# Optimization experiments

Hardware: AMD Instinct MI355X
Metric: run time of the kernel (lower is better)

## Reference

```python
import jax, jax.numpy as jnp
import numpy as np

VOCAB = 32000
EMBED = 256
UNITS = 1024
BATCH = 16
SEQ = 128


def setup_inputs() -> dict:
    key = jax.random.key(0)
    ks = jax.random.split(key, 7)
    scale_in = 1.0 / np.sqrt(EMBED + UNITS)
    return {
        "inputs": jax.random.randint(ks[0], (BATCH, SEQ), 0, VOCAB, dtype=jnp.int64),
        "emb": jax.random.normal(ks[1], (VOCAB, EMBED), dtype=jnp.float32) * 0.05,
        "W": jax.random.normal(ks[2], (EMBED, 4 * UNITS), dtype=jnp.float32) * scale_in,
        "U": jax.random.normal(ks[3], (UNITS, 4 * UNITS), dtype=jnp.float32) * scale_in,
        "b": jnp.zeros((4 * UNITS,), dtype=jnp.float32),
        "Wc": jax.random.normal(ks[5], (UNITS, VOCAB), dtype=jnp.float32) * (1.0 / np.sqrt(UNITS)),
        "bc": jnp.zeros((VOCAB,), dtype=jnp.float32),
    }


def reference(inputs, emb, W, U, b, Wc, bc):
    # Embedding lookup: [B, T] -> [B, T, E]
    x = emb[inputs]
    B, T, E = x.shape
    H = U.shape[0]

    def step(carry, xt):
        h, c = carry
        # fused gate pre-activations: [B, 4H]
        z = xt @ W + h @ U + b
        i, f, g, o = jnp.split(z, 4, axis=-1)
        c_new = jax.nn.sigmoid(f) * c + jax.nn.sigmoid(i) * jnp.tanh(g)
        h_new = jax.nn.sigmoid(o) * jnp.tanh(c_new)
        return (h_new, c_new), h_new

    h0 = jnp.zeros((B, H), dtype=x.dtype)
    c0 = jnp.zeros((B, H), dtype=x.dtype)
    (h, c), hs = jax.lax.scan(step, (h0, c0), jnp.swapaxes(x, 0, 1))  # hs: [T, B, H]

    out = jnp.swapaxes(hs, 0, 1).reshape(-1, H)  # [B*T, H]
    logits = out @ Wc + bc                        # [B*T, vocab]
    return logits
```

## Files before the change

### kernel.cpp

```cpp
#include <hip/hip_runtime.h>
#include <hip/hip_bf16.h>
#include <math.h>


#define VOCAB 32000
#define EMBED 256
#define UNITS 1024
#define GATES 4096
#define BATCH 16
#define SEQ 128
#define NB 64

using s16x8 = __attribute__((ext_vector_type(8))) short;
using f16x8 = __attribute__((ext_vector_type(8))) _Float16;
using f32x4 = __attribute__((ext_vector_type(4))) float;

__device__ __forceinline__ unsigned short f16_bits(float x) {
    _Float16 h = (_Float16)x;
    return __builtin_bit_cast(unsigned short, h);
}
__device__ __forceinline__ float f16_f32(unsigned short b) {
    return (float)__builtin_bit_cast(_Float16, b);
}
__device__ __forceinline__ int swz_e(int r, int k) {
    return (r * 64 + k) ^ ((((r & 7) ^ ((r >> 2) & 7))) << 3);
}
__device__ __forceinline__ unsigned long long ld_u64(const unsigned long long* p) {
    return __hip_atomic_load(p, __ATOMIC_RELAXED, __HIP_MEMORY_SCOPE_AGENT);
}
__device__ __forceinline__ unsigned poison_u64(unsigned long long v) {
    return (unsigned)((unsigned)v == 0xFFFFFFFFu) |
           (unsigned)((unsigned)(v >> 32) == 0xFFFFFFFFu);
}

__global__ void __launch_bounds__(256) k_prep(
    const float* __restrict__ U,
    unsigned short* __restrict__ ub_hi,
    unsigned short* __restrict__ ub_lo,
    const int* __restrict__ inputs,
    const float* __restrict__ emb,
    const float* __restrict__ W,
    const float* __restrict__ bias,
    float* __restrict__ xWb) {
    __shared__ __align__(16) char smem_raw[65536];
    const int tid = threadIdx.x;

    if (blockIdx.x < 256) {
        float* lds_u = (float*)smem_raw;
        const int ct = blockIdx.x;
        for (int k = tid; k < 1024; k += 256) {
            const float4* src = (const float4*)(U + (size_t)k * GATES + ct * 16);
            float4* dst = (float4*)(&lds_u[k * 16]);
            dst[0] = src[0]; dst[1] = src[1]; dst[2] = src[2]; dst[3] = src[3];
        }
        __syncthreads();
        const int lane = tid & 63;
        const int coll = lane & 15;
        const int kg = lane >> 4;
        for (int kt = (tid >> 6); kt < 32; kt += 4) {
            const int ks = kt * 32 + kg * 8;
            unsigned short h8[8], l8[8];
#pragma unroll
            for (int e = 0; e < 8; ++e) {
                float v = lds_u[(ks + e) * 16 + coll];
                unsigned short hb = f16_bits(v);
                h8[e] = hb;
                l8[e] = f16_bits(v - f16_f32(hb));
            }
            size_t o = (((size_t)ct * 32 + kt) * 64 + lane) * 8;
            *(s16x8*)(ub_hi + o) = *(const s16x8*)h8;
            *(s16x8*)(ub_lo + o) = *(const s16x8*)l8;
        }
        return;
    }

    const int eb = blockIdx.x - 256;
    const int t   = eb >> 4;
    const int col = (eb & 15) * 256 + tid;
    float (*xs)[EMBED] = (float (*)[EMBED])smem_raw;
    int* toks = (int*)(smem_raw + 16384);
    if (tid < BATCH)
        toks[tid] = inputs[tid * SEQ + t];
    __syncthreads();
    for (int r = 0; r < BATCH; ++r)
        xs[r][tid] = emb[(size_t)toks[r] * EMBED + tid];
    __syncthreads();
    float acc[BATCH];
#pragma unroll
    for (int r = 0; r < BATCH; ++r) acc[r] = 0.f;
    for (int k0 = 0; k0 < EMBED; k0 += 4) {
        float4 xv[BATCH];
#pragma unroll
        for (int r = 0; r < BATCH; ++r)
            xv[r] = *(const float4*)(&xs[r][k0]);
#pragma unroll
        for (int e = 0; e < 4; ++e) {
            float w = W[(size_t)(k0 + e) * GATES + col];
#pragma unroll
            for (int r = 0; r < BATCH; ++r)
                acc[r] += ((const float*)&xv[r])[e] * w;
        }
    }
    const float bb = bias[col];
#pragma unroll
    for (int r = 0; r < BATCH; ++r)
        xWb[((size_t)t * BATCH + r) * GATES + col] = acc[r] + bb;
}

__global__ void __launch_bounds__(512, 2) k_fused(
    const unsigned short* __restrict__ ub_hi,
    const unsigned short* __restrict__ ub_lo,
    const float* __restrict__ xWb,
    unsigned short* __restrict__ hsl,
    const float* __restrict__ Wc,
    const float* __restrict__ bc,
    float* __restrict__ out) {
    __shared__ __align__(16) char smem_raw[32768];
    const int tid  = threadIdx.x;
    const int lane = tid & 63;
    const int w    = tid >> 6;

    if (blockIdx.x < NB) {
        __builtin_amdgcn_s_setprio(1);
        float (*zpart)[4][256] = (float (*)[4][256])smem_raw;
        const int bid = blockIdx.x;
        const int j0  = bid * 16;

        const int b_own  = (tid >> 4) & 15;
        const int jj_own = tid & 15;
        const int j_own  = j0 + jj_own;
        const int hb_e = ((j_own >> 5) * 512) + (((j_own >> 3) & 3) * 16 + b_own) * 8 + (j_own & 7);
        float c_own = 0.f;

        f16x8 Uh[4][4], Ul[4][4];
#pragma unroll
        for (int g = 0; g < 4; ++g)
#pragma unroll
            for (int q = 0; q < 4; ++q) {
                size_t o = (((size_t)(g * 64 + bid) * 32) + (w * 4 + q)) * 512 + lane * 8;
                Uh[g][q] = *(const f16x8*)(ub_hi + o);
                Ul[g][q] = *(const f16x8*)(ub_lo + o);
            }

        for (int t = 0; t < SEQ; ++t) {
            float xw0 = 0.f, xw1 = 0.f, xw2 = 0.f, xw3 = 0.f;
            if (tid < 256) {
                const float* xwp = xWb + ((size_t)t * BATCH + b_own) * GATES + j_own;
                xw0 = xwp[0]; xw1 = xwp[UNITS]; xw2 = xwp[2 * UNITS]; xw3 = xwp[3 * UNITS];
            }

            const unsigned long long* p64 =
                (const unsigned long long*)(hsl + (size_t)t * 32768);

            union HU { unsigned long long q2[2]; f16x8 v; };
            HU hh[4], hl[4];
            while (true) {
                unsigned bad = 0;
#pragma unroll
                for (int q = 0; q < 4; ++q) {
                    const size_t u = (size_t)(w * 4 + q) * 128 + lane * 2;
                    hh[q].q2[0] = ld_u64(p64 + u);
                    hh[q].q2[1] = ld_u64(p64 + u + 1);
                    hl[q].q2[0] = ld_u64(p64 + 4096 + u);
                    hl[q].q2[1] = ld_u64(p64 + 4097 + u);
                }
#pragma unroll
                for (int q = 0; q < 4; ++q)
                    bad |= poison_u64(hh[q].q2[0]) | poison_u64(hh[q].q2[1]) |
                           poison_u64(hl[q].q2[0]) | poison_u64(hl[q].q2[1]);
                if (__all((int)(bad == 0))) break;
                __builtin_amdgcn_s_sleep(8);
            }

            f32x4 a0[4], a1[4], a2[4];
#pragma unroll
            for (int g = 0; g < 4; ++g) {
                a0[g] = (f32x4){0.f, 0.f, 0.f, 0.f};
                a1[g] = (f32x4){0.f, 0.f, 0.f, 0.f};
                a2[g] = (f32x4){0.f, 0.f, 0.f, 0.f};
            }
#pragma unroll
            for (int q = 0; q < 4; ++q)
#pragma unroll
                for (int g = 0; g < 4; ++g) {
                    a0[g] = __builtin_amdgcn_mfma_f32_16x16x32_f16(hh[q].v, Uh[g][q], a0[g], 0, 0, 0);
                    a1[g] = __builtin_amdgcn_mfma_f32_16x16x32_f16(hh[q].v, Ul[g][q], a1[g], 0, 0, 0);
                    a2[g] = __builtin_amdgcn_mfma_f32_16x16x32_f16(hl[q].v, Uh[g][q], a2[g], 0, 0, 0);
                }

#pragma unroll
            for (int g = 0; g < 4; ++g)
#pragma unroll
                for (int r = 0; r < 4; ++r)
                    zpart[w][g][((lane >> 4) * 4 + r) * 16 + (lane & 15)] =
                        a0[g][r] + a1[g][r] + a2[g][r];
            __syncthreads();

            if (tid < 256) {
                const int zi_idx = b_own * 16 + jj_own;
                float zi = xw0, zf = xw1, zg = xw2, zo = xw3;
#pragma unroll
                for (int ww = 0; ww < 8; ++ww) {
                    zi += zpart[ww][0][zi_idx];
                    zf += zpart[ww][1][zi_idx];
                    zg += zpart[ww][2][zi_idx];
                    zo += zpart[ww][3][zi_idx];
                }
                float si = 1.f / (1.f + expf(-zi));
                float sf = 1.f / (1.f + expf(-zf));
                float so = 1.f / (1.f + expf(-zo));
                float c_new = sf * c_own + si * tanhf(zg);
                float h_new = so * tanhf(c_new);
                c_own = c_new;

                int hhi = (int)f16_bits(h_new);
                int hlo = (int)f16_bits(h_new - f16_f32((unsigned short)hhi));
                int hhi_nb = __shfl_xor(hhi, 1);
                int hlo_nb = __shfl_xor(hlo, 1);
                unsigned short* nh = hsl + (size_t)(t + 1) * 32768;
                if ((tid & 1) == 0) {
                    unsigned hp = (unsigned)(unsigned short)hhi | ((unsigned)(unsigned short)hhi_nb << 16);
                    unsigned lp = (unsigned)(unsigned short)hlo | ((unsigned)(unsigned short)hlo_nb << 16);
                    __hip_atomic_store((unsigned*)(nh + hb_e), hp,
                                       __ATOMIC_RELAXED, __HIP_MEMORY_SCOPE_AGENT);
                    __hip_atomic_store((unsigned*)(nh + 16384 + hb_e), lp,
                                       __ATOMIC_RELAXED, __HIP_MEMORY_SCOPE_AGENT);
                }
            }
        }
        return;
    }

    unsigned short* Bs = (unsigned short*)smem_raw;
    const int bidp = blockIdx.x - NB;
    const int mt2 = bidp / 250;
    const int nt  = bidp % 250;
    const int n0 = nt * 128;

    {
        const unsigned long long* gp =
            (const unsigned long long*)(hsl + (size_t)(mt2 * 8 + 8) * 32768);
        {
            const unsigned long long* sp = gp + (size_t)tid * 8;
            unsigned long long v = ld_u64(sp);
            while (poison_u64(v)) {
                __builtin_amdgcn_s_sleep(32);
                v = ld_u64(sp);
            }
        }
        while (true) {
            unsigned bad = 0;
#pragma unroll
            for (int i = 0; i < 8; ++i)
                bad |= poison_u64(ld_u64(gp + (size_t)i * 512 + tid));
            if (__syncthreads_and((int)(bad == 0))) break;
            __builtin_amdgcn_s_sleep(16);
        }
        asm volatile("" ::: "memory");
    }

    const int b_kb  = (tid >> 5) * 8;
    const int b_nb4 = (tid & 31) * 4;
    const int wmt  = (w >> 2) * 4;
    const int wn   = (w & 3) * 32;
    const int lr   = lane & 15;
    const int kg   = lane >> 4;

    f32x4 acc[4][2];
#pragma unroll
    for (int i = 0; i < 4; ++i)
#pragma unroll
        for (int j = 0; j < 2; ++j) acc[i][j] = (f32x4){0.f, 0.f, 0.f, 0.f};

    const unsigned short* aslot[4];
#pragma unroll
    for (int mi = 0; mi < 4; ++mi)
        aslot[mi] = hsl + (size_t)(mt2 * 8 + wmt + mi + 1) * 32768 + lane * 8;

    f16x8 A0h[4], A1h[4];
#pragma unroll
    for (int mi = 0; mi < 4; ++mi) {
        A0h[mi] = *(const f16x8*)(aslot[mi]);
        A1h[mi] = *(const f16x8*)(aslot[mi] + 512);
    }
    float4 rawB[8];
    if (tid < 256) {
#pragma unroll
        for (int i = 0; i < 8; ++i)
            rawB[i] = *(const float4*)(Wc + (size_t)(b_kb + i) * VOCAB + n0 + b_nb4);
    }

    for (int kt = 0; kt < 16; ++kt) {
        __syncthreads();
        if (tid < 256) {
#pragma unroll
            for (int nn = 0; nn < 4; ++nn) {
                unsigned short h8[8];
#pragma unroll
                for (int i = 0; i < 8; ++i)
                    h8[i] = f16_bits(((const float*)&rawB[i])[nn]);
                int e = swz_e(b_nb4 + nn, b_kb);
                *(s16x8*)(&Bs[e]) = *(const s16x8*)h8;
            }
        }
        __syncthreads();
        if (kt < 15 && tid < 256) {
            const int k0n = (kt + 1) * 64;
#pragma unroll
            for (int i = 0; i < 8; ++i)
                rawB[i] = *(const float4*)(Wc + (size_t)(k0n + b_kb + i) * VOCAB + n0 + b_nb4);
        }
        {
            f16x8 bh[2];
#pragma unroll
            for (int ni = 0; ni < 2; ++ni)
                bh[ni] = *(const f16x8*)(&Bs[swz_e(wn + ni * 16 + lr, kg * 8)]);
#pragma unroll
            for (int mi = 0; mi < 4; ++mi)
#pragma unroll
                for (int ni = 0; ni < 2; ++ni)
                    acc[mi][ni] = __builtin_amdgcn_mfma_f32_16x16x32_f16(A0h[mi], bh[ni], acc[mi][ni], 0, 0, 0);
            if (kt < 15) {
                const int base = (kt + 1) * 1024;
#pragma unroll
                for (int mi = 0; mi < 4; ++mi)
                    A0h[mi] = *(const f16x8*)(aslot[mi] + base);
            }
        }
        {
            f16x8 bh[2];
#pragma unroll
            for (int ni = 0; ni < 2; ++ni)
                bh[ni] = *(const f16x8*)(&Bs[swz_e(wn + ni * 16 + lr, 32 + kg * 8)]);
#pragma unroll
            for (int mi = 0; mi < 4; ++mi)
#pragma unroll
                for (int ni = 0; ni < 2; ++ni)
                    acc[mi][ni] = __builtin_amdgcn_mfma_f32_16x16x32_f16(A1h[mi], bh[ni], acc[mi][ni], 0, 0, 0);
            if (kt < 15) {
                const int base = (kt + 1) * 1024 + 512;
#pragma unroll
                for (int mi = 0; mi < 4; ++mi)
                    A1h[mi] = *(const f16x8*)(aslot[mi] + base);
            }
        }
    }

    float bcv[2];
#pragma unroll
    for (int ni = 0; ni < 2; ++ni) bcv[ni] = bc[n0 + wn + ni * 16 + lr];
#pragma unroll
    for (int mi = 0; mi < 4; ++mi) {
        const int trow = mt2 * 8 + wmt + mi;
#pragma unroll
        for (int ni = 0; ni < 2; ++ni) {
#pragma unroll
            for (int r = 0; r < 4; ++r) {
                int grow = (kg * 4 + r) * 128 + trow;
                int gcol = n0 + wn + ni * 16 + lr;
                __builtin_nontemporal_store(acc[mi][ni][r] + bcv[ni],
                                            &out[(size_t)grow * VOCAB + gcol]);
            }
        }
    }
}

extern "C" void kernel_launch(void* const* d_in, const int* in_sizes, int n_in,
                              void* d_out, int out_size, void* d_ws, size_t ws_size,
                              hipStream_t stream) {
    const int*   inputs = (const int*)d_in[0];
    const float* emb  = (const float*)d_in[1];
    const float* W    = (const float*)d_in[2];
    const float* U    = (const float*)d_in[3];
    const float* bias = (const float*)d_in[4];
    const float* Wc   = (const float*)d_in[5];
    const float* bc   = (const float*)d_in[6];
    float* out = (float*)d_out;

    char* ws = (char*)d_ws;
    float*          xWb   = (float*)(ws + 0);
    unsigned short* ub_hi = (unsigned short*)(ws + 33554432);
    unsigned short* ub_lo = (unsigned short*)(ws + 41943040);
    unsigned short* hsl   = (unsigned short*)(ws + 50331648);

    hipMemsetAsync(hsl, 0, 65536, stream);
    hipMemsetAsync((char*)hsl + 65536, 0xFF, 8454144 - 65536, stream);

    k_prep<<<256 + 2048, 256, 0, stream>>>(U, ub_hi, ub_lo,
                                           inputs, emb, W, bias, xWb);
    k_fused<<<NB + 4000, 512, 0, stream>>>(ub_hi, ub_lo, xWb, hsl, Wc, bc, out);
}
```

Measured before the change: 733.1 us.

## Move input projection into fused kernel with per-timestep ready flags

The embedding lookup and x@W+b projection move out of the prep kernel and into new block roles inside the persistent fused kernel. Each block publishes a per-timestep, per-column-slice flag after its stores drain. The recurrent blocks poll these flags alongside the hidden-state poison check before reading xWb. The aim is to overlap the input projection with the recurrence and shrink the prep kernel to just the U split, at the cost of extra polling and added scheduling dependence among co-resident blocks.

```diff
diff --git a/kernel.cpp b/kernel.cpp
--- a/kernel.cpp
+++ b/kernel.cpp
@@ -10,6 +10,7 @@
 #define BATCH 16
 #define SEQ 128
 #define NB 64
+#define EMB_BLKS 1024
 
 using s16x8 = __attribute__((ext_vector_type(8))) short;
 using f16x8 = __attribute__((ext_vector_type(8))) _Float16;
@@ -28,90 +29,59 @@
 __device__ __forceinline__ unsigned long long ld_u64(const unsigned long long* p) {
     return __hip_atomic_load(p, __ATOMIC_RELAXED, __HIP_MEMORY_SCOPE_AGENT);
 }
+__device__ __forceinline__ unsigned ld_u32(const unsigned* p) {
+    return __hip_atomic_load(p, __ATOMIC_RELAXED, __HIP_MEMORY_SCOPE_AGENT);
+}
+__device__ __forceinline__ void st_u32(unsigned* p, unsigned v) {
+    __hip_atomic_store(p, v, __ATOMIC_RELAXED, __HIP_MEMORY_SCOPE_AGENT);
+}
 __device__ __forceinline__ unsigned poison_u64(unsigned long long v) {
     return (unsigned)((unsigned)v == 0xFFFFFFFFu) |
            (unsigned)((unsigned)(v >> 32) == 0xFFFFFFFFu);
 }
 
-__global__ void __launch_bounds__(256) k_prep(
+__global__ void __launch_bounds__(256) k_prep_u(
     const float* __restrict__ U,
     unsigned short* __restrict__ ub_hi,
-    unsigned short* __restrict__ ub_lo,
+    unsigned short* __restrict__ ub_lo) {
+    __shared__ float lds_u[1024 * 16];
+    const int ct = blockIdx.x;
+    const int tid = threadIdx.x;
+    for (int k = tid; k < 1024; k += 256) {
+        const float4* src = (const float4*)(U + (size_t)k * GATES + ct * 16);
+        float4* dst = (float4*)(&lds_u[k * 16]);
+        dst[0] = src[0]; dst[1] = src[1]; dst[2] = src[2]; dst[3] = src[3];
+    }
+    __syncthreads();
+    const int lane = tid & 63;
+    const int coll = lane & 15;
+    const int kg = lane >> 4;
+    for (int kt = (tid >> 6); kt < 32; kt += 4) {
+        const int ks = kt * 32 + kg * 8;
+        unsigned short h8[8], l8[8];
+#pragma unroll
+        for (int e = 0; e < 8; ++e) {
+            float v = lds_u[(ks + e) * 16 + coll];
+            unsigned short hb = f16_bits(v);
+            h8[e] = hb;
+            l8[e] = f16_bits(v - f16_f32(hb));
+        }
+        size_t o = (((size_t)ct * 32 + kt) * 64 + lane) * 8;
+        *(s16x8*)(ub_hi + o) = *(const s16x8*)h8;
+        *(s16x8*)(ub_lo + o) = *(const s16x8*)l8;
+    }
+}
+
+__global__ void __launch_bounds__(512, 2) k_fused(
+    const unsigned short* __restrict__ ub_hi,
+    const unsigned short* __restrict__ ub_lo,
+    float* __restrict__ xWb,
+    unsigned short* __restrict__ hsl,
+    unsigned* __restrict__ xwf,
     const int* __restrict__ inputs,
     const float* __restrict__ emb,
     const float* __restrict__ W,
     const float* __restrict__ bias,
-    float* __restrict__ xWb) {
-    __shared__ __align__(16) char smem_raw[65536];
-    const int tid = threadIdx.x;
-
-    if (blockIdx.x < 256) {
-        float* lds_u = (float*)smem_raw;
-        const int ct = blockIdx.x;
-        for (int k = tid; k < 1024; k += 256) {
-            const float4* src = (const float4*)(U + (size_t)k * GATES + ct * 16);
-            float4* dst = (float4*)(&lds_u[k * 16]);
-            dst[0] = src[0]; dst[1] = src[1]; dst[2] = src[2]; dst[3] = src[3];
-        }
-        __syncthreads();
-        const int lane = tid & 63;
-        const int coll = lane & 15;
-        const int kg = lane >> 4;
-        for (int kt = (tid >> 6); kt < 32; kt += 4) {
-            const int ks = kt * 32 + kg * 8;
-            unsigned short h8[8], l8[8];
-#pragma unroll
-            for (int e = 0; e < 8; ++e) {
-                float v = lds_u[(ks + e) * 16 + coll];
-                unsigned short hb = f16_bits(v);
-                h8[e] = hb;
-                l8[e] = f16_bits(v - f16_f32(hb));
-            }
-            size_t o = (((size_t)ct * 32 + kt) * 64 + lane) * 8;
-            *(s16x8*)(ub_hi + o) = *(const s16x8*)h8;
-            *(s16x8*)(ub_lo + o) = *(const s16x8*)l8;
-        }
-        return;
-    }
-
-    const int eb = blockIdx.x - 256;
-    const int t   = eb >> 4;
-    const int col = (eb & 15) * 256 + tid;
-    float (*xs)[EMBED] = (float (*)[EMBED])smem_raw;
-    int* toks = (int*)(smem_raw + 16384);
-    if (tid < BATCH)
-        toks[tid] = inputs[tid * SEQ + t];
-    __syncthreads();
-    for (int r = 0; r < BATCH; ++r)
-        xs[r][tid] = emb[(size_t)toks[r] * EMBED + tid];
-    __syncthreads();
-    float acc[BATCH];
-#pragma unroll
-    for (int r = 0; r < BATCH; ++r) acc[r] = 0.f;
-    for (int k0 = 0; k0 < EMBED; k0 += 4) {
-        float4 xv[BATCH];
-#pragma unroll
-        for (int r = 0; r < BATCH; ++r)
-            xv[r] = *(const float4*)(&xs[r][k0]);
-#pragma unroll
-        for (int e = 0; e < 4; ++e) {
-            float w = W[(size_t)(k0 + e) * GATES + col];
-#pragma unroll
-            for (int r = 0; r < BATCH; ++r)
-                acc[r] += ((const float*)&xv[r])[e] * w;
-        }
-    }
-    const float bb = bias[col];
-#pragma unroll
-    for (int r = 0; r < BATCH; ++r)
-        xWb[((size_t)t * BATCH + r) * GATES + col] = acc[r] + bb;
-}
-
-__global__ void __launch_bounds__(512, 2) k_fused(
-    const unsigned short* __restrict__ ub_hi,
-    const unsigned short* __restrict__ ub_lo,
-    const float* __restrict__ xWb,
-    unsigned short* __restrict__ hsl,
     const float* __restrict__ Wc,
     const float* __restrict__ bc,
     float* __restrict__ out) {
@@ -143,19 +113,15 @@
             }
 
         for (int t = 0; t < SEQ; ++t) {
-            float xw0 = 0.f, xw1 = 0.f, xw2 = 0.f, xw3 = 0.f;
-            if (tid < 256) {
-                const float* xwp = xWb + ((size_t)t * BATCH + b_own) * GATES + j_own;
-                xw0 = xwp[0]; xw1 = xwp[UNITS]; xw2 = xwp[2 * UNITS]; xw3 = xwp[3 * UNITS];
-            }
-
             const unsigned long long* p64 =
                 (const unsigned long long*)(hsl + (size_t)t * 32768);
+            const unsigned* xwfp = xwf + t * 8;
 
             union HU { unsigned long long q2[2]; f16x8 v; };
             HU hh[4], hl[4];
             while (true) {
-                unsigned bad = 0;
+                unsigned fl = ld_u32(&xwfp[lane & 7]);
+                unsigned bad = (unsigned)(fl == 0u);
 #pragma unroll
                 for (int q = 0; q < 4; ++q) {
                     const size_t u = (size_t)(w * 4 + q) * 128 + lane * 2;
@@ -170,6 +136,13 @@
                            poison_u64(hl[q].q2[0]) | poison_u64(hl[q].q2[1]);
                 if (__all((int)(bad == 0))) break;
                 __builtin_amdgcn_s_sleep(8);
+            }
+            asm volatile("" ::: "memory");
+
+            float xw0 = 0.f, xw1 = 0.f, xw2 = 0.f, xw3 = 0.f;
+            if (tid < 256) {
+                const float* xwp = xWb + ((size_t)t * BATCH + b_own) * GATES + j_own;
+                xw0 = xwp[0]; xw1 = xwp[UNITS]; xw2 = xwp[2 * UNITS]; xw3 = xwp[3 * UNITS];
             }
 
             f32x4 a0[4], a1[4], a2[4];
@@ -221,18 +194,56 @@
                 if ((tid & 1) == 0) {
                     unsigned hp = (unsigned)(unsigned short)hhi | ((unsigned)(unsigned short)hhi_nb << 16);
                     unsigned lp = (unsigned)(unsigned short)hlo | ((unsigned)(unsigned short)hlo_nb << 16);
-                    __hip_atomic_store((unsigned*)(nh + hb_e), hp,
-                                       __ATOMIC_RELAXED, __HIP_MEMORY_SCOPE_AGENT);
-                    __hip_atomic_store((unsigned*)(nh + 16384 + hb_e), lp,
-                                       __ATOMIC_RELAXED, __HIP_MEMORY_SCOPE_AGENT);
+                    st_u32((unsigned*)(nh + hb_e), hp);
+                    st_u32((unsigned*)(nh + 16384 + hb_e), lp);
                 }
             }
         }
         return;
     }
 
+    if (blockIdx.x < NB + EMB_BLKS) {
+        const int eb  = blockIdx.x - NB;
+        const int t   = eb >> 3;
+        const int col = (eb & 7) * 512 + tid;
+        float (*xs)[EMBED] = (float (*)[EMBED])smem_raw;
+        int* toks = (int*)(smem_raw + 16384);
+        if (tid < BATCH)
+            toks[tid] = inputs[tid * SEQ + t];
+        __syncthreads();
+        for (int i = tid; i < BATCH * EMBED; i += 512)
+            xs[i >> 8][i & 255] = emb[(size_t)toks[i >> 8] * EMBED + (i & 255)];
+        __syncthreads();
+        float acc[BATCH];
+#pragma unroll
+        for (int r = 0; r < BATCH; ++r) acc[r] = 0.f;
+        for (int k0 = 0; k0 < EMBED; k0 += 4) {
+            float4 xv[BATCH];
+#pragma unroll
+            for (int r = 0; r < BATCH; ++r)
+                xv[r] = *(const float4*)(&xs[r][k0]);
+#pragma unroll
+            for (int e = 0; e < 4; ++e) {
+                float wv = W[(size_t)(k0 + e) * GATES + col];
+#pragma unroll
+                for (int r = 0; r < BATCH; ++r)
+                    acc[r] += ((const float*)&xv[r])[e] * wv;
+            }
+        }
+        const float bb = bias[col];
+#pragma unroll
+        for (int r = 0; r < BATCH; ++r)
+            st_u32((unsigned*)&xWb[((size_t)t * BATCH + r) * GATES + col],
+                   __builtin_bit_cast(unsigned, acc[r] + bb));
+        asm volatile("s_waitcnt vmcnt(0)" ::: "memory");
+        __syncthreads();
+        if (tid == 0)
+            st_u32(&xwf[t * 8 + (eb & 7)], 1u);
+        return;
+    }
+
     unsigned short* Bs = (unsigned short*)smem_raw;
-    const int bidp = blockIdx.x - NB;
+    const int bidp = blockIdx.x - NB - EMB_BLKS;
     const int mt2 = bidp / 250;
     const int nt  = bidp % 250;
     const int n0 = nt * 128;
@@ -382,11 +393,13 @@
     unsigned short* ub_hi = (unsigned short*)(ws + 33554432);
     unsigned short* ub_lo = (unsigned short*)(ws + 41943040);
     unsigned short* hsl   = (unsigned short*)(ws + 50331648);
+    unsigned*       xwf   = (unsigned*)(ws + 58785792);
 
     hipMemsetAsync(hsl, 0, 65536, stream);
     hipMemsetAsync((char*)hsl + 65536, 0xFF, 8454144 - 65536, stream);
-
-    k_prep<<<256 + 2048, 256, 0, stream>>>(U, ub_hi, ub_lo,
-                                           inputs, emb, W, bias, xWb);
-    k_fused<<<NB + 4000, 512, 0, stream>>>(ub_hi, ub_lo, xWb, hsl, Wc, bc, out);
-}
+    hipMemsetAsync(xwf, 0, 4096, stream);
+
+    k_prep_u<<<256, 256, 0, stream>>>(U, ub_hi, ub_lo);
+    k_fused<<<NB + EMB_BLKS + 4000, 512, 0, stream>>>(
+        ub_hi, ub_lo, xWb, hsl, xwf, inputs, emb, W, bias, Wc, bc, out);
+}
```

Result: no change. 740.4 us (+1.0%).
